# Kernel tuning notes

Measured on AMD Instinct MI355X. Metric: run time of the kernel, lower is better.

The kernel has to match this reference:

```python
import jax, jax.numpy as jnp
import numpy as np

THRESHOLD = 33.33  # torch forward default

def setup_inputs() -> dict:
    key = jax.random.key(0)
    k1, k2 = jax.random.split(key)
    source_pc = jax.random.normal(k1, (2, 16384, 3), dtype=jnp.float32)
    target_pc = jax.random.normal(k2, (2, 16384, 3), dtype=jnp.float32)
    return {"source_pc": source_pc, "target_pc": target_pc}

def _pairwise_dist(x, y):
    # Euclidean cdist via the matmul expansion (same math as torch.cdist p=2).
    # x: [B, N, D], y: [B, M, D] -> [B, N, M]
    x2 = jnp.sum(x * x, axis=-1)              # [B, N]
    y2 = jnp.sum(y * y, axis=-1)              # [B, M]
    xy = jnp.einsum('bnd,bmd->bnm', x, y)     # [B, N, M]
    d2 = x2[:, :, None] + y2[None if False else slice(None), None, :] - 2.0 * xy
    d2 = x2[:, :, None] + y2[:, None, :] - 2.0 * xy
    return jnp.sqrt(jnp.maximum(d2, 0.0))

def reference(source_pc, target_pc):
    dist = _pairwise_dist(source_pc.astype(jnp.float32), target_pc.astype(jnp.float32))
    dist1 = jnp.minimum(jnp.min(dist, axis=2), THRESHOLD)  # [B, N] clamped
    dist2 = jnp.minimum(jnp.min(dist, axis=1), THRESHOLD)  # [B, M] clamped
    d1 = jnp.mean(dist1, axis=-1)
    d2 = jnp.mean(dist2, axis=-1)
    return (d1 + d2) / 2.0  # bidirectional=True default -> [B]
```

## Files before the change

kernel.cpp:

```cpp
#include <hip/hip_runtime.h>

#define NPTS 16384
#define TH 33.33f

typedef __attribute__((ext_vector_type(8)))  __bf16 bf16x8;
typedef __attribute__((ext_vector_type(16))) float  f32x16;
typedef __attribute__((ext_vector_type(16))) unsigned u32x16;

__device__ __forceinline__ unsigned short f2bf(float x) {
    unsigned u = __float_as_uint(x);
    u += 0x7FFFu + ((u >> 16) & 1u);
    return (unsigned short)(u >> 16);
}
__device__ __forceinline__ float bf2f(unsigned short h) {
    return __uint_as_float(((unsigned)h) << 16);
}
__device__ __forceinline__ unsigned umin_(unsigned a, unsigned b) { return a < b ? a : b; }

union UV { uint4 v; bf16x8 h; unsigned short s[8]; };


#define FOLD2(MM, AA) { \
    f32x16 t0 = __builtin_amdgcn_mfma_f32_32x32x16_bf16(AA, q0, zc, 0, 0, 0); \
    f32x16 t1 = __builtin_amdgcn_mfma_f32_32x32x16_bf16(AA, q1, zc, 0, 0, 0); \
    _Pragma("unroll") for (int j = 0; j < 16; j++) \
        MM[j] = umin_(umin_(__float_as_uint(t0[j]), __float_as_uint(t1[j])), MM[j]); }

__device__ __forceinline__ void conv_store(unsigned short* lb, int k,
                                           float x, float y, float z) {
    float hp = 0.5f * fmaf(z, z, fmaf(y, y, x * x));
    unsigned short xh = f2bf(x), yh = f2bf(y), zh = f2bf(z);
    unsigned short xl = f2bf(x - bf2f(xh)), yl = f2bf(y - bf2f(yh)), zl = f2bf(z - bf2f(zh));
    float rr = hp;
    unsigned short h0 = f2bf(rr); rr -= bf2f(h0);
    unsigned short h1 = f2bf(rr); rr -= bf2f(h1);
    unsigned short h2 = f2bf(rr);
    UV c0, c1;
    c0.s[0]=xh; c0.s[1]=yh; c0.s[2]=zh; c0.s[3]=xh; c0.s[4]=yh; c0.s[5]=zh; c0.s[6]=xl; c0.s[7]=yl;
    c1.s[0]=zl; c1.s[1]=(unsigned short)(h0^0x8000); c1.s[2]=(unsigned short)(h1^0x8000);
    c1.s[3]=(unsigned short)(h2^0x8000);
    c1.s[4]=0xC200;
    c1.s[5]=0; c1.s[6]=0; c1.s[7]=0;
    int t = k >> 5, pos = k & 31;
    *(uint4*)(lb + t * 512 + pos * 8)       = c0.v;
    *(uint4*)(lb + t * 512 + 256 + pos * 8) = c1.v;
}

#define LOAD_PTS(CC) { \
    const float* g0 = pp + (size_t)(seg * 2048 + (CC) * 512 + tid) * 3; \
    px0 = g0[0]; py0 = g0[1]; pz0 = g0[2]; \
    const float* g1 = g0 + 768; \
    px1 = g1[0]; py1 = g1[1]; pz1 = g1[2]; }

#define CONV_WRITE(BUF) { \
    unsigned short* lb = (unsigned short*)(smem + (BUF) * 16384); \
    conv_store(lb, tid,       px0, py0, pz0); \
    conv_store(lb, tid + 256, px1, py1, pz1); }

#define EPILOG(MM, P) { \
    unsigned* sc = scratch + wave * 1056; \
    _Pragma("unroll") for (int j = 0; j < 16; j++) { \
        int r0 = (j & 3) + 8 * (j >> 2) + 4 * g; sc[r0 * 33 + cc] = MM[j]; } \
    __syncthreads(); \
    const unsigned* sr = sc + cc * 33 + g * 16; \
    unsigned mx = 0xFF800000u; \
    _Pragma("unroll") for (int k = 0; k < 16; k++) mx = umin_(mx, sr[k]); \
    mx = umin_(mx, (unsigned)__shfl_xor((int)mx, 32, 64)); \
    if (lane < 32) { \
        float sbi = __uint_as_float(mx); \
        float d2 = 2.0f * (hq[P] - 32.0f - sbi); \
        float d = fminf(sqrtf(fmaxf(d2, 0.0f)), TH); \
        dst[wave * 64 + (P) * 32 + lane] = d; } \
    __syncthreads(); }

__global__ __launch_bounds__(256, 5) void chamfer_kernel(
        const float* __restrict__ src, const float* __restrict__ tgt,
        float* __restrict__ d2part, float* __restrict__ out)
{
    const int db = blockIdx.y, dir = db >> 1, b = db & 1;
    const int rowblock = blockIdx.x >> 3, seg = blockIdx.x & 7;
    const int tid = threadIdx.x, wave = tid >> 6, lane = tid & 63;
    const int g = lane >> 5, cc = lane & 31;
    if (blockIdx.x == 0 && db == 0 && tid < 2) out[tid] = 0.0f;
    const float* qp = (dir == 0 ? src : tgt) + (size_t)b * NPTS * 3;
    const float* pp = (dir == 0 ? tgt : src) + (size_t)b * NPTS * 3;
    const unsigned short one = 0x3F80;

    __shared__ alignas(16) unsigned char smem[32768];
    unsigned* scratch = (unsigned*)smem;

    const int rt0 = rowblock * 8 + wave * 2;
    bf16x8 afrag[2]; float hq[2];
#pragma unroll
    for (int i = 0; i < 2; i++) {
        int r = (rt0 + i) * 32 + cc;
        float x = qp[r * 3 + 0], y = qp[r * 3 + 1], z = qp[r * 3 + 2];
        hq[i] = 0.5f * fmaf(z, z, fmaf(y, y, x * x));
        unsigned short xh = f2bf(x), yh = f2bf(y), zh = f2bf(z);
        unsigned short xl = f2bf(x - bf2f(xh)), yl = f2bf(y - bf2f(yh)), zl = f2bf(z - bf2f(zh));
        UV f0, f1, rv;
        f0.s[0]=xh; f0.s[1]=yh; f0.s[2]=zh; f0.s[3]=xl; f0.s[4]=yl; f0.s[5]=zl; f0.s[6]=xh; f0.s[7]=yh;
        f1.s[0]=zh; f1.s[1]=one; f1.s[2]=one; f1.s[3]=one;
        f1.s[4]=one;
        f1.s[5]=0; f1.s[6]=0; f1.s[7]=0;
        rv.v = g ? f1.v : f0.v;
        afrag[i] = rv.h;
    }

    u32x16 m0 = 0xFF800000u, m1 = 0xFF800000u;
    const f32x16 zc = 0.0f;
    float px0, py0, pz0, px1, py1, pz1;

    LOAD_PTS(0)
    CONV_WRITE(0)
    __syncthreads();
#pragma unroll 1
    for (int c = 0; c < 4; ++c) {
        if (c < 3) LOAD_PTS(c + 1)
        const unsigned short* bb = (const unsigned short*)(smem + (c & 1) * 16384);
#pragma unroll 1
        for (int pt = 0; pt < 8; ++pt) {
            bf16x8 q0 = *(const bf16x8*)(bb + pt * 1024 + lane * 8);
            bf16x8 q1 = *(const bf16x8*)(bb + pt * 1024 + 512 + lane * 8);
            FOLD2(m0, afrag[0])
            FOLD2(m1, afrag[1])
        }
        if (c < 3) CONV_WRITE((c + 1) & 1)
        __syncthreads();
    }

    float* dst = d2part + (((size_t)(db * 64 + rowblock)) * 8 + seg) * 256;
    EPILOG(m0, 0)
    EPILOG(m1, 1)
}

__global__ __launch_bounds__(256) void merge_kernel(const float* __restrict__ d2part,
                                                    float* __restrict__ out) {
    const int b = blockIdx.y;
    const int slice = blockIdx.x;
    const int tid = threadIdx.x;
    float s = 0.0f;
#pragma unroll
    for (int pass = 0; pass < 2; pass++) {
        const float* base = d2part + (size_t)(pass * 2 + b) * 64 * 8 * 256;
#pragma unroll
        for (int i = 0; i < 4; i++) {
            int r = slice * 1024 + i * 256 + tid;
            const float* p = base + (size_t)(r >> 8) * 2048 + (r & 255);
            float m = p[0];
#pragma unroll
            for (int sgi = 1; sgi < 8; sgi++) m = fminf(m, p[sgi * 256]);
            s += m;
        }
    }
#pragma unroll
    for (int off = 32; off > 0; off >>= 1) s += __shfl_down(s, off, 64);
    __shared__ float w[4];
    if ((tid & 63) == 0) w[tid >> 6] = s;
    __syncthreads();
    if (tid == 0) {
        float t = (w[0] + w[1]) + (w[2] + w[3]);
        atomicAdd(&out[b], t * (1.0f / (2.0f * NPTS)));
    }
}

extern "C" void kernel_launch(void* const* d_in, const int* in_sizes, int n_in,
                              void* d_out, int out_size, void* d_ws, size_t ws_size,
                              hipStream_t stream) {
    const float* src = (const float*)d_in[0];
    const float* tgt = (const float*)d_in[1];
    float* out = (float*)d_out;
    float* d2part = (float*)d_ws;

    chamfer_kernel<<<dim3(512, 4), 256, 0, stream>>>(src, tgt, d2part, out);
    merge_kernel<<<dim3(16, 2), 256, 0, stream>>>(d2part, out);
}
```

Before: 96.87 us.

## Precompute bf16 point fragments in a prep kernel and halve rows per block

Result: no change. 96.68 us (-0.2%).

```diff
diff --git a/kernel.cpp b/kernel.cpp
--- a/kernel.cpp
+++ b/kernel.cpp
@@ -20,14 +20,18 @@
 union UV { uint4 v; bf16x8 h; unsigned short s[8]; };
 
 
-#define FOLD2(MM, AA) { \
-    f32x16 t0 = __builtin_amdgcn_mfma_f32_32x32x16_bf16(AA, q0, zc, 0, 0, 0); \
-    f32x16 t1 = __builtin_amdgcn_mfma_f32_32x32x16_bf16(AA, q1, zc, 0, 0, 0); \
-    _Pragma("unroll") for (int j = 0; j < 16; j++) \
-        MM[j] = umin_(umin_(__float_as_uint(t0[j]), __float_as_uint(t1[j])), MM[j]); }
+__global__ __launch_bounds__(256) void prep_kernel(
+        const float* __restrict__ src, const float* __restrict__ tgt,
+        unsigned char* __restrict__ pfmt, float* __restrict__ out)
+{
+    const int set = blockIdx.y;
+    const int chunk = blockIdx.x;
+    const int tid = threadIdx.x;
+    if (set == 0 && chunk == 0 && tid < 2) out[tid] = 0.0f;
+    const float* base = (set < 2 ? src : tgt) + (size_t)(set & 1) * NPTS * 3;
+    const int p = chunk * 256 + tid;
+    const float x = base[p * 3 + 0], y = base[p * 3 + 1], z = base[p * 3 + 2];
 
-__device__ __forceinline__ void conv_store(unsigned short* lb, int k,
-                                           float x, float y, float z) {
     float hp = 0.5f * fmaf(z, z, fmaf(y, y, x * x));
     unsigned short xh = f2bf(x), yh = f2bf(y), zh = f2bf(z);
     unsigned short xl = f2bf(x - bf2f(xh)), yl = f2bf(y - bf2f(yh)), zl = f2bf(z - bf2f(zh));
@@ -41,61 +45,35 @@
     c1.s[3]=(unsigned short)(h2^0x8000);
     c1.s[4]=0xC200;
     c1.s[5]=0; c1.s[6]=0; c1.s[7]=0;
-    int t = k >> 5, pos = k & 31;
-    *(uint4*)(lb + t * 512 + pos * 8)       = c0.v;
-    *(uint4*)(lb + t * 512 + 256 + pos * 8) = c1.v;
+
+    unsigned char* ob = pfmt + (size_t)set * NPTS * 32
+                             + (size_t)(p >> 5) * 1024 + (size_t)(p & 31) * 16;
+    *(uint4*)(ob)       = c0.v;
+    *(uint4*)(ob + 512) = c1.v;
 }
 
-#define LOAD_PTS(CC) { \
-    const float* g0 = pp + (size_t)(seg * 2048 + (CC) * 512 + tid) * 3; \
-    px0 = g0[0]; py0 = g0[1]; pz0 = g0[2]; \
-    const float* g1 = g0 + 768; \
-    px1 = g1[0]; py1 = g1[1]; pz1 = g1[2]; }
-
-#define CONV_WRITE(BUF) { \
-    unsigned short* lb = (unsigned short*)(smem + (BUF) * 16384); \
-    conv_store(lb, tid,       px0, py0, pz0); \
-    conv_store(lb, tid + 256, px1, py1, pz1); }
-
-#define EPILOG(MM, P) { \
-    unsigned* sc = scratch + wave * 1056; \
-    _Pragma("unroll") for (int j = 0; j < 16; j++) { \
-        int r0 = (j & 3) + 8 * (j >> 2) + 4 * g; sc[r0 * 33 + cc] = MM[j]; } \
-    __syncthreads(); \
-    const unsigned* sr = sc + cc * 33 + g * 16; \
-    unsigned mx = 0xFF800000u; \
-    _Pragma("unroll") for (int k = 0; k < 16; k++) mx = umin_(mx, sr[k]); \
-    mx = umin_(mx, (unsigned)__shfl_xor((int)mx, 32, 64)); \
-    if (lane < 32) { \
-        float sbi = __uint_as_float(mx); \
-        float d2 = 2.0f * (hq[P] - 32.0f - sbi); \
-        float d = fminf(sqrtf(fmaxf(d2, 0.0f)), TH); \
-        dst[wave * 64 + (P) * 32 + lane] = d; } \
-    __syncthreads(); }
-
-__global__ __launch_bounds__(256, 5) void chamfer_kernel(
+__global__ __launch_bounds__(256, 8) void chamfer_kernel(
         const float* __restrict__ src, const float* __restrict__ tgt,
-        float* __restrict__ d2part, float* __restrict__ out)
+        const unsigned char* __restrict__ pfmt, float* __restrict__ d2part)
 {
     const int db = blockIdx.y, dir = db >> 1, b = db & 1;
     const int rowblock = blockIdx.x >> 3, seg = blockIdx.x & 7;
     const int tid = threadIdx.x, wave = tid >> 6, lane = tid & 63;
     const int g = lane >> 5, cc = lane & 31;
-    if (blockIdx.x == 0 && db == 0 && tid < 2) out[tid] = 0.0f;
     const float* qp = (dir == 0 ? src : tgt) + (size_t)b * NPTS * 3;
-    const float* pp = (dir == 0 ? tgt : src) + (size_t)b * NPTS * 3;
+    const int pset = (dir == 0 ? 2 + b : b);
+    const unsigned char* ps = pfmt + (size_t)pset * NPTS * 32 + (size_t)seg * 2048 * 32;
     const unsigned short one = 0x3F80;
 
-    __shared__ alignas(16) unsigned char smem[32768];
+    __shared__ alignas(16) unsigned char smem[16896];
     unsigned* scratch = (unsigned*)smem;
 
-    const int rt0 = rowblock * 8 + wave * 2;
-    bf16x8 afrag[2]; float hq[2];
-#pragma unroll
-    for (int i = 0; i < 2; i++) {
-        int r = (rt0 + i) * 32 + cc;
+    const int rt = rowblock * 4 + wave;
+    bf16x8 afrag; float hq;
+    {
+        int r = rt * 32 + cc;
         float x = qp[r * 3 + 0], y = qp[r * 3 + 1], z = qp[r * 3 + 2];
-        hq[i] = 0.5f * fmaf(z, z, fmaf(y, y, x * x));
+        hq = 0.5f * fmaf(z, z, fmaf(y, y, x * x));
         unsigned short xh = f2bf(x), yh = f2bf(y), zh = f2bf(z);
         unsigned short xl = f2bf(x - bf2f(xh)), yl = f2bf(y - bf2f(yh)), zl = f2bf(z - bf2f(zh));
         UV f0, f1, rv;
@@ -104,34 +82,62 @@
         f1.s[4]=one;
         f1.s[5]=0; f1.s[6]=0; f1.s[7]=0;
         rv.v = g ? f1.v : f0.v;
-        afrag[i] = rv.h;
+        afrag = rv.h;
     }
 
-    u32x16 m0 = 0xFF800000u, m1 = 0xFF800000u;
+    u32x16 m0 = 0xFF800000u;
     const f32x16 zc = 0.0f;
-    float px0, py0, pz0, px1, py1, pz1;
 
-    LOAD_PTS(0)
-    CONV_WRITE(0)
+    {
+        const uint4* gsrc = (const uint4*)ps + tid * 4;
+        uint4 a0 = gsrc[0], a1 = gsrc[1], a2 = gsrc[2], a3 = gsrc[3];
+        uint4* lw = (uint4*)smem + tid * 4;
+        lw[0] = a0; lw[1] = a1; lw[2] = a2; lw[3] = a3;
+    }
     __syncthreads();
 #pragma unroll 1
     for (int c = 0; c < 4; ++c) {
-        if (c < 3) LOAD_PTS(c + 1)
-        const unsigned short* bb = (const unsigned short*)(smem + (c & 1) * 16384);
+        const unsigned short* bb = (const unsigned short*)smem;
 #pragma unroll 1
         for (int pt = 0; pt < 8; ++pt) {
             bf16x8 q0 = *(const bf16x8*)(bb + pt * 1024 + lane * 8);
             bf16x8 q1 = *(const bf16x8*)(bb + pt * 1024 + 512 + lane * 8);
-            FOLD2(m0, afrag[0])
-            FOLD2(m1, afrag[1])
+            f32x16 t0 = __builtin_amdgcn_mfma_f32_32x32x16_bf16(afrag, q0, zc, 0, 0, 0);
+            f32x16 t1 = __builtin_amdgcn_mfma_f32_32x32x16_bf16(afrag, q1, zc, 0, 0, 0);
+#pragma unroll
+            for (int j = 0; j < 16; j++)
+                m0[j] = umin_(umin_(__float_as_uint(t0[j]), __float_as_uint(t1[j])), m0[j]);
         }
-        if (c < 3) CONV_WRITE((c + 1) & 1)
+        __syncthreads();
+        if (c < 3) {
+            const uint4* gsrc = (const uint4*)(ps + (size_t)(c + 1) * 16384) + tid * 4;
+            uint4 a0 = gsrc[0], a1 = gsrc[1], a2 = gsrc[2], a3 = gsrc[3];
+            uint4* lw = (uint4*)smem + tid * 4;
+            lw[0] = a0; lw[1] = a1; lw[2] = a2; lw[3] = a3;
+        }
         __syncthreads();
     }
 
-    float* dst = d2part + (((size_t)(db * 64 + rowblock)) * 8 + seg) * 256;
-    EPILOG(m0, 0)
-    EPILOG(m1, 1)
+    float* dst = d2part + (((size_t)(db * 128 + rowblock)) * 8 + seg) * 128;
+    {
+        unsigned* sc = scratch + wave * 1056;
+#pragma unroll
+        for (int j = 0; j < 16; j++) {
+            int r0 = (j & 3) + 8 * (j >> 2) + 4 * g;
+            sc[r0 * 33 + cc] = m0[j];
+        }
+        const unsigned* sr = sc + cc * 33 + g * 16;
+        unsigned mx = 0xFF800000u;
+#pragma unroll
+        for (int k = 0; k < 16; k++) mx = umin_(mx, sr[k]);
+        mx = umin_(mx, (unsigned)__shfl_xor((int)mx, 32, 64));
+        if (lane < 32) {
+            float sbi = __uint_as_float(mx);
+            float d2 = 2.0f * (hq - 32.0f - sbi);
+            float d = fminf(sqrtf(fmaxf(d2, 0.0f)), TH);
+            dst[wave * 32 + lane] = d;
+        }
+    }
 }
 
 __global__ __launch_bounds__(256) void merge_kernel(const float* __restrict__ d2part,
@@ -142,14 +148,14 @@
     float s = 0.0f;
 #pragma unroll
     for (int pass = 0; pass < 2; pass++) {
-        const float* base = d2part + (size_t)(pass * 2 + b) * 64 * 8 * 256;
+        const float* base = d2part + (size_t)(pass * 2 + b) * 128 * 8 * 128;
 #pragma unroll
         for (int i = 0; i < 4; i++) {
             int r = slice * 1024 + i * 256 + tid;
-            const float* p = base + (size_t)(r >> 8) * 2048 + (r & 255);
+            const float* p = base + (size_t)(r >> 7) * 1024 + (r & 127);
             float m = p[0];
 #pragma unroll
-            for (int sgi = 1; sgi < 8; sgi++) m = fminf(m, p[sgi * 256]);
+            for (int sgi = 1; sgi < 8; sgi++) m = fminf(m, p[sgi * 128]);
             s += m;
         }
     }
@@ -170,8 +176,10 @@
     const float* src = (const float*)d_in[0];
     const float* tgt = (const float*)d_in[1];
     float* out = (float*)d_out;
-    float* d2part = (float*)d_ws;
+    unsigned char* pfmt = (unsigned char*)d_ws;
+    float* d2part = (float*)(pfmt + (size_t)4 * 1024 * 1024);
 
-    chamfer_kernel<<<dim3(512, 4), 256, 0, stream>>>(src, tgt, d2part, out);
+    prep_kernel<<<dim3(64, 4), 256, 0, stream>>>(src, tgt, pfmt, out);
+    chamfer_kernel<<<dim3(1024, 4), 256, 0, stream>>>(src, tgt, pfmt, d2part);
     merge_kernel<<<dim3(16, 2), 256, 0, stream>>>(d2part, out);
 }
```
